# Performance work log

Hardware: AMD Instinct MI355X
Metric: run time of the kernel (lower is better)

The kernel has to match this reference:

```python
import jax, jax.numpy as jnp
import numpy as np

THRESH_LOW = 0.90
THRESH_HIGH = 0.95
IOU_THRESH = 0.05
IOU_LOW = 0.1


def _interp1d(size, dtype):
    # roi_align sample offsets for a 4-wide box, bin=4, grid=ceil(4/1)=4:
    # center + (i+0.5)*1 - 2 -> {-1.5,-0.5,0.5,1.5}
    offs = jnp.array([-1.5, -0.5, 0.5, 1.5], dtype)
    c = jnp.arange(size, dtype=dtype)[:, None] + offs  # [size,4]
    valid = (c >= -1.0) & (c <= size)  # torchvision: zero if y < -1 or y > H
    cc = jnp.clip(c, 0.0, size - 1.0)
    lo = jnp.floor(cc).astype(jnp.int32)
    hi = jnp.minimum(lo + 1, size - 1)
    frac = cc - lo.astype(dtype)
    w_lo = jnp.where(valid, 1.0 - frac, 0.0)
    w_hi = jnp.where(valid, frac, 0.0)
    return lo, hi, w_lo, w_hi


def _roi_pool(m):
    # roi_align(output_size=1, spatial_scale=1, sampling_ratio=-1, aligned=False)
    # over one 4x4 anchor per pixel: separable bilinear gather, mean of 16 samples.
    H, W = m.shape
    ylo, yhi, wy0, wy1 = _interp1d(H, m.dtype)
    xlo, xhi, wx0, wx1 = _interp1d(W, m.dtype)
    A = jnp.einsum('hkw,hk->hw', m[ylo], wy0) + jnp.einsum('hkw,hk->hw', m[yhi], wy1)
    B = jnp.einsum('hwk,wk->hw', A[:, xlo], wx0) + jnp.einsum('hwk,wk->hw', A[:, xhi], wx1)
    return B / 16.0


def _anchors(H, W, dtype):
    # torchvision AnchorGenerator(sizes=(5,), aspects=(1.0,)): base anchor
    # round([-2.5,-2.5,2.5,2.5]) = [-2,-2,2,2]; stride 1; x fastest, y outer.
    yy, xx = jnp.meshgrid(jnp.arange(H, dtype=dtype), jnp.arange(W, dtype=dtype), indexing='ij')
    a = jnp.stack([xx - 2.0, yy - 2.0, xx + 2.0, yy + 2.0], axis=-1)
    return a.reshape(-1, 4)


def _iou_one_vs_all(box, boxes):
    lt = jnp.maximum(box[:2], boxes[:, :2])
    rb = jnp.minimum(box[2:], boxes[:, 2:])
    wh = jnp.maximum(rb - lt, 0.0)
    inter = wh[:, 0] * wh[:, 1]
    area1 = (box[2] - box[0]) * (box[3] - box[1])
    area2 = (boxes[:, 2] - boxes[:, 0]) * (boxes[:, 3] - boxes[:, 1])
    return inter / (area1 + area2 - inter)


def _nms(boxes, scores, thr):
    # Greedy NMS (torchvision semantics: suppress IoU > thr), returns kept
    # indices sorted by descending score. Row-wise IoU avoids an MxM matrix.
    M = boxes.shape[0]
    if M == 0:
        return jnp.zeros((0,), jnp.int32)
    order = jnp.argsort(-scores)
    b = boxes[order]
    rng = jnp.arange(M)
    def body(i, keep):
        sup = (_iou_one_vs_all(b[i], b) > thr) & (rng > i) & keep[i]
        return keep & ~sup
    keep = jax.lax.fori_loop(0, M, body, jnp.ones((M,), bool))
    return order[keep]


def _logits(x1, x2, x3):
    r = (jnp.abs(x1 - x2).sum(axis=1) + jnp.abs(x2 - x3).sum(axis=1)) / 2.0  # [B,H,W]
    rmax = r.reshape(r.shape[0], -1).max(axis=-1)[:, None, None]
    rmin = r.reshape(r.shape[0], -1).min(axis=-1)[:, None, None]
    r = (r - rmin) / (rmax - rmin + 1e-6)
    m = r[0]  # B == 1
    logits = _roi_pool(m).reshape(-1)  # [H*W], row-major (y outer, x inner)
    return logits / (logits.max() + 1e-6)


def setup_inputs():
    key = jax.random.key(0)
    k1, k2, k3 = jax.random.split(key, 3)
    shape = (1, 8, 1024, 1024)
    return {
        'x1': jax.random.normal(k1, shape, jnp.float32),
        'x2': jax.random.normal(k2, shape, jnp.float32),
        'x3': jax.random.normal(k3, shape, jnp.float32),
    }


def reference(x1, x2, x3):
    H, W = x1.shape[-2:]
    anchors = _anchors(H, W, x1.dtype)
    logits = _logits(x1, x2, x3)
    idx = jnp.arange(logits.shape[0])
    # low band, NMS @ 0.1
    idx_low = idx[(logits > THRESH_LOW) & (logits < THRESH_HIGH)]
    idx_low = idx_low[_nms(anchors[idx_low], logits[idx_low], IOU_LOW)]
    # high band, NMS @ iou_thresh
    idx_high = idx[logits > THRESH_HIGH]
    idx_high = idx_high[_nms(anchors[idx_high], logits[idx_high], IOU_THRESH)]
    # combined NMS
    idx_cat = jnp.concatenate([idx_high, idx_low])
    idx_final = idx_cat[_nms(anchors[idx_cat], logits[idx_cat], IOU_THRESH)]
    return jnp.concatenate([anchors[idx_final], logits[idx_final][:, None]], axis=-1)
```

## Files before the change

### kernel.cpp

```cpp
#include <hip/hip_runtime.h>
#include <stdint.h>

#define GW 1024
#define GH 1024
#define NPIX (GW*GH)
#define CAP 8192
#define KCAP 4096
#define ADJ_STRIDE 48

__global__ void k_resid(const float4* __restrict__ x1, const float4* __restrict__ x2,
                        const float4* __restrict__ x3, float4* __restrict__ r,
                        float2* __restrict__ pmm) {
  const int N4 = NPIX / 4;
  int t = blockIdx.x * blockDim.x + threadIdx.x;
  float4 s1 = make_float4(0.f,0.f,0.f,0.f);
  float4 s2 = make_float4(0.f,0.f,0.f,0.f);
#pragma unroll
  for (int c = 0; c < 8; ++c) {
    float4 a = x1[c*N4 + t];
    float4 b = x2[c*N4 + t];
    float4 d = x3[c*N4 + t];
    s1.x += fabsf(a.x-b.x); s1.y += fabsf(a.y-b.y);
    s1.z += fabsf(a.z-b.z); s1.w += fabsf(a.w-b.w);
    s2.x += fabsf(b.x-d.x); s2.y += fabsf(b.y-d.y);
    s2.z += fabsf(b.z-d.z); s2.w += fabsf(b.w-d.w);
  }
  float4 rv = make_float4((s1.x+s2.x)*0.5f, (s1.y+s2.y)*0.5f,
                          (s1.z+s2.z)*0.5f, (s1.w+s2.w)*0.5f);
  r[t] = rv;
  float mn = fminf(fminf(rv.x,rv.y), fminf(rv.z,rv.w));
  float mx = fmaxf(fmaxf(rv.x,rv.y), fmaxf(rv.z,rv.w));
#pragma unroll
  for (int o = 32; o > 0; o >>= 1) {
    mn = fminf(mn, __shfl_down(mn, o));
    mx = fmaxf(mx, __shfl_down(mx, o));
  }
  __shared__ float smn[4], smx[4];
  int wid = threadIdx.x >> 6;
  if ((threadIdx.x & 63) == 0) { smn[wid] = mn; smx[wid] = mx; }
  __syncthreads();
  if (threadIdx.x == 0) {
    float a = fminf(fminf(smn[0], smn[1]), fminf(smn[2], smn[3]));
    float b = fmaxf(fmaxf(smx[0], smx[1]), fmaxf(smx[2], smx[3]));
    pmm[blockIdx.x] = make_float2(a, b);
  }
}

__global__ __launch_bounds__(1024) void k_reduce1(const float2* __restrict__ pmm,
                                                  unsigned int* __restrict__ mm) {
  int t = threadIdx.x;
  float2 p = pmm[t];
  float mn = p.x, mx = p.y;
#pragma unroll
  for (int o = 32; o > 0; o >>= 1) {
    mn = fminf(mn, __shfl_down(mn, o));
    mx = fmaxf(mx, __shfl_down(mx, o));
  }
  __shared__ float smn[16], smx[16];
  int wid = t >> 6;
  if ((t & 63) == 0) { smn[wid] = mn; smx[wid] = mx; }
  __syncthreads();
  if (t == 0) {
    mn = smn[0]; mx = smx[0];
#pragma unroll
    for (int i = 1; i < 16; ++i) { mn = fminf(mn, smn[i]); mx = fmaxf(mx, smx[i]); }
    mm[1] = __float_as_uint(mn);
    mm[2] = __float_as_uint(mx);
  }
}

__global__ void k_convy(const float* __restrict__ r, float* __restrict__ A,
                        const unsigned int* __restrict__ mm) {
  int x = blockIdx.x * 256 + threadIdx.x;
  int y = blockIdx.y;
  float rmin = __uint_as_float(mm[1]);
  float denom = __uint_as_float(mm[2]) - rmin + 1e-6f;
  const float offs[4] = {-1.5f, -0.5f, 0.5f, 1.5f};
  float a = 0.f, b = 0.f;
#pragma unroll
  for (int k = 0; k < 4; ++k) {
    float c = (float)y + offs[k];
    bool valid = (c >= -1.0f) && (c <= (float)GH);
    float cc = fminf(fmaxf(c, 0.0f), (float)(GH - 1));
    int lo = (int)floorf(cc);
    int hi = min(lo + 1, GH - 1);
    float frac = cc - (float)lo;
    float w0 = valid ? 1.0f - frac : 0.0f;
    float w1 = valid ? frac : 0.0f;
    a += ((r[lo*GW + x] - rmin) / denom) * w0;
    b += ((r[hi*GW + x] - rmin) / denom) * w1;
  }
  A[y*GW + x] = a + b;
}

__global__ void k_convx(const float* __restrict__ A, float* __restrict__ B,
                        float* __restrict__ pbmax) {
  __shared__ float sA[GW];
  __shared__ float smx[4];
  int y = blockIdx.x, t = threadIdx.x;
  ((float4*)sA)[t] = ((const float4*)(A + (size_t)y*GW))[t];
  __syncthreads();
  const float offs[4] = {-1.5f, -0.5f, 0.5f, 1.5f};
  float mxv = 0.0f;
#pragma unroll
  for (int q = 0; q < 4; ++q) {
    int x = t + 256*q;
    float a = 0.f, b = 0.f;
#pragma unroll
    for (int k = 0; k < 4; ++k) {
      float c = (float)x + offs[k];
      bool valid = (c >= -1.0f) && (c <= (float)GW);
      float cc = fminf(fmaxf(c, 0.0f), (float)(GW - 1));
      int lo = (int)floorf(cc);
      int hi = min(lo + 1, GW - 1);
      float frac = cc - (float)lo;
      float w0 = valid ? 1.0f - frac : 0.0f;
      float w1 = valid ? frac : 0.0f;
      a += sA[lo] * w0;
      b += sA[hi] * w1;
    }
    float v = (a + b) * 0.0625f;
    B[(size_t)y*GW + x] = v;
    mxv = fmaxf(mxv, v);
  }
#pragma unroll
  for (int o = 32; o > 0; o >>= 1) mxv = fmaxf(mxv, __shfl_down(mxv, o));
  int wid = t >> 6;
  if ((t & 63) == 0) smx[wid] = mxv;
  __syncthreads();
  if (t == 0)
    pbmax[y] = fmaxf(fmaxf(smx[0], smx[1]), fmaxf(smx[2], smx[3]));
}

__global__ __launch_bounds__(1024) void k_reduce2(const float* __restrict__ pbmax,
                                                  unsigned int* __restrict__ mm) {
  int t = threadIdx.x;
  float mx = pbmax[t];
#pragma unroll
  for (int o = 32; o > 0; o >>= 1) mx = fmaxf(mx, __shfl_down(mx, o));
  __shared__ float smx[16];
  int wid = t >> 6;
  if ((t & 63) == 0) smx[wid] = mx;
  __syncthreads();
  if (t == 0) {
    mx = smx[0];
#pragma unroll
    for (int i = 1; i < 16; ++i) mx = fmaxf(mx, smx[i]);
    mm[3] = __float_as_uint(mx);
    mm[0] = 0u;
  }
}

__global__ void k_cand(const float4* __restrict__ B, uint4* __restrict__ map,
                       unsigned int* __restrict__ list, float* __restrict__ scores,
                       unsigned int* __restrict__ mm) {
  int t = blockIdx.x * 256 + threadIdx.x;
  int tid = threadIdx.x;
  float bmax = __uint_as_float(mm[3]);
  float dv = bmax + 1e-6f;
  float4 b = B[t];
  float l[4] = { b.x/dv, b.y/dv, b.z/dv, b.w/dv };
  unsigned int flags = 0; int cnt = 0;
#pragma unroll
  for (int k = 0; k < 4; ++k) {
    float s = l[k];
    if (s > 0.90f && !(s == 0.95f)) { flags |= 1u << k; cnt++; }
  }
  __shared__ unsigned int sscan[256];
  __shared__ unsigned int sbase;
  sscan[tid] = (unsigned int)cnt;
  __syncthreads();
  for (int off = 1; off < 256; off <<= 1) {
    unsigned int v = sscan[tid];
    unsigned int a = (tid >= off) ? sscan[tid - off] : 0u;
    __syncthreads();
    sscan[tid] = v + a;
    __syncthreads();
  }
  if (tid == 255) {
    unsigned int tot = sscan[255];
    if (tot) sbase = atomicAdd(&mm[0], tot);
  }
  __syncthreads();
  unsigned int mv[4] = { ~0u, ~0u, ~0u, ~0u };
  if (flags) {
    unsigned int o = sbase + sscan[tid] - (unsigned int)cnt;
    unsigned int base4 = (unsigned int)t * 4u;
#pragma unroll
    for (int k = 0; k < 4; ++k) {
      if ((flags >> k) & 1u) {
        if (o < CAP) { list[o] = base4 + (unsigned int)k; scores[o] = l[k]; mv[k] = o; }
        o++;
      }
    }
  }
  map[t] = make_uint4(mv[0], mv[1], mv[2], mv[3]);
}

__global__ void k_adj(const unsigned int* __restrict__ list,
                      const float* __restrict__ scores,
                      const unsigned int* __restrict__ map,
                      const unsigned int* __restrict__ mm,
                      unsigned short* __restrict__ adj) {
  int r = blockIdx.x * 256 + threadIdx.x;
  int M = (int)min(mm[0], (unsigned int)CAP);
  if (r >= M) return;
  unsigned int pos = list[r];
  float s = scores[r];
  unsigned int sb = __float_as_uint(s);
  unsigned int high = (s > 0.95f) ? 1u : 0u;
  int y = (int)(pos >> 10), x = (int)(pos & 1023);
  int n = 0, n3 = 0;
  unsigned short* row = adj + (size_t)r * ADJ_STRIDE;
#pragma unroll
  for (int pass = 0; pass < 2; ++pass) {
    for (int dy = -3; dy <= 3; ++dy) {
      int ady = dy < 0 ? -dy : dy;
      int wy = 4 - ady;
      int ny = y + dy;
      if ((unsigned)ny >= (unsigned)GH) continue;
      for (int dx = -3; dx <= 3; ++dx) {
        if ((dx | dy) == 0) continue;
        int adx = dx < 0 ? -dx : dx;
        int prod = (4 - adx) * wy;
        if (prod < 2) continue;
        if ((pass == 0) != (prod >= 3)) continue;
        int nx = x + dx;
        if ((unsigned)nx >= (unsigned)GW) continue;
        unsigned int npix = (unsigned int)(ny*GW + nx);
        unsigned int nid = map[npix];
        if (nid == ~0u) continue;
        float ns = scores[nid];
        unsigned int nsb = __float_as_uint(ns);
        if (nsb > sb || (nsb == sb && npix < pos)) {
          unsigned int nh = (ns > 0.95f) ? 1u : 0u;
          row[1 + n] = (unsigned short)(nid | (nh << 15));
          n++;
          if (pass == 0) n3++;
        }
      }
    }
  }
  row[0] = (unsigned short)(n3 | (n << 6) | (high << 12));
}

__global__ __launch_bounds__(1024) void k_nms(const unsigned int* __restrict__ list,
                                              const float* __restrict__ scores,
                                              const unsigned short* __restrict__ adj,
                                              const unsigned int* __restrict__ mm,
                                              float* __restrict__ out, int nrows) {
  __shared__ unsigned char st[CAP];
  __shared__ unsigned short act[2][CAP];
  __shared__ unsigned long long skeys[KCAP];
  __shared__ unsigned int s_cnt[2];
  __shared__ unsigned int s_k;
  const int tid = threadIdx.x;
  int M = (int)min(mm[0], (unsigned int)CAP);
  for (int i = tid; i < CAP; i += 1024) st[i] = 0;
  for (int i = tid; i < M; i += 1024) act[0][i] = (unsigned short)i;
  if (tid == 0) { s_cnt[0] = (unsigned int)M; s_cnt[1] = 0; s_k = 0; }
  __syncthreads();

  int cur = 0;
  for (int round = 0; round < CAP; ++round) {
    unsigned int cnt = s_cnt[cur];
    if (cnt == 0) break;
    for (unsigned int i = tid; i < cnt; i += 1024) {
      int r = act[cur][i];
      const unsigned short* row = adj + (size_t)r * ADJ_STRIDE;
      unsigned int hdr = row[0];
      unsigned int high = (hdr >> 12) & 1u;
      int n = high ? (int)((hdr >> 6) & 63u) : (int)(hdr & 63u);
      unsigned char lowbit = high ? 0 : 16;
      bool sup = false, und = false;
      for (int k = 1; k <= n; ++k) {
        unsigned int e = row[k];
        if (((e >> 15) & 1u) != high) continue;
        unsigned char ps = st[e & 0x1FFFu];
        if (ps & 2) { sup = true; break; }
        if (!(ps & 1)) und = true;
      }
      if (sup)          st[r] = (unsigned char)(1 | lowbit);
      else if (!und)    st[r] = (unsigned char)(3 | lowbit);
      else { unsigned int j = atomicAdd(&s_cnt[cur ^ 1], 1u); act[cur ^ 1][j] = (unsigned short)r; }
    }
    __syncthreads();
    if (tid == 0) s_cnt[cur] = 0;
    cur ^= 1;
    __syncthreads();
  }
  __syncthreads();

  if (tid == 0) { s_cnt[0] = 0; s_cnt[1] = 0; }
  __syncthreads();
  for (int i = tid; i < M; i += 1024) {
    unsigned char s0 = st[i];
    if ((s0 & 16) && (s0 & 2)) {
      unsigned int j = atomicAdd(&s_cnt[0], 1u); act[0][j] = (unsigned short)i;
    }
  }
  __syncthreads();
  cur = 0;
  for (int round = 0; round < CAP; ++round) {
    unsigned int cnt = s_cnt[cur];
    if (cnt == 0) break;
    for (unsigned int i = tid; i < cnt; i += 1024) {
      int r = act[cur][i];
      const unsigned short* row = adj + (size_t)r * ADJ_STRIDE;
      unsigned int hdr = row[0];
      int n = (int)((hdr >> 6) & 63u);
      bool sup = false, und = false;
      for (int k = 1; k <= n; ++k) {
        unsigned int e = row[k];
        unsigned char ps = st[e & 0x1FFFu];
        if ((e >> 15) & 1u) {
          if (ps & 2) { sup = true; break; }
        } else {
          if (!(ps & 2)) continue;
          if (ps & 8) { sup = true; break; }
          if (!(ps & 4)) und = true;
        }
      }
      if (sup)          st[r] |= 4;
      else if (!und)    st[r] |= 12;
      else { unsigned int j = atomicAdd(&s_cnt[cur ^ 1], 1u); act[cur ^ 1][j] = (unsigned short)r; }
    }
    __syncthreads();
    if (tid == 0) s_cnt[cur] = 0;
    cur ^= 1;
    __syncthreads();
  }
  __syncthreads();

  for (int i = tid; i < M; i += 1024) {
    unsigned char s0 = st[i];
    bool keep = (s0 & 16) ? ((s0 & 8) != 0) : ((s0 & 2) != 0);
    if (keep) {
      unsigned int j = atomicAdd(&s_k, 1u);
      if (j < KCAP) {
        unsigned int pos = list[i];
        unsigned int sb = __float_as_uint(scores[i]);
        skeys[j] = (((unsigned long long)(0xFFFFFFFFu - sb)) << 32) | (unsigned long long)pos;
      }
    }
  }
  __syncthreads();
  unsigned int K = min(s_k, (unsigned int)KCAP);

  for (unsigned int i = tid; i < K; i += 1024) {
    unsigned long long key = skeys[i];
    unsigned int rank = 0;
    for (unsigned int q = 0; q < K; ++q) rank += (skeys[q] < key) ? 1u : 0u;
    if ((int)rank < nrows) {
      unsigned int pos = (unsigned int)(key & 0xFFFFFFFFu);
      float s = __uint_as_float(0xFFFFFFFFu - (unsigned int)(key >> 32));
      float fx = (float)(pos & 1023), fy = (float)(pos >> 10);
      out[rank*5 + 0] = fx - 2.0f;
      out[rank*5 + 1] = fy - 2.0f;
      out[rank*5 + 2] = fx + 2.0f;
      out[rank*5 + 3] = fy + 2.0f;
      out[rank*5 + 4] = s;
    }
  }
}

extern "C" void kernel_launch(void* const* d_in, const int* in_sizes, int n_in,
                              void* d_out, int out_size, void* d_ws, size_t ws_size,
                              hipStream_t stream) {
  const float* x1 = (const float*)d_in[0];
  const float* x2 = (const float*)d_in[1];
  const float* x3 = (const float*)d_in[2];
  char* ws = (char*)d_ws;
  float* rmap = (float*)ws;
  float* Amap = (float*)(ws + (4u << 20));
  float* Bmap = (float*)(ws + (8u << 20));
  unsigned int* map = (unsigned int*)(ws + (4u << 20));
  unsigned int* mm  = (unsigned int*)(ws + (12u << 20));
  unsigned int* list = (unsigned int*)(ws + (12u << 20) + 4096u);
  float* scores = (float*)(ws + (12u << 20) + (64u << 10));
  unsigned short* adj = (unsigned short*)(ws + (12u << 20) + (128u << 10));
  float2* pmm = (float2*)(ws + (13u << 20));
  float* pbmax = (float*)(ws + (13u << 20) + (16u << 10));
  float* out = (float*)d_out;

  k_resid<<<NPIX/4/256, 256, 0, stream>>>((const float4*)x1, (const float4*)x2,
                                          (const float4*)x3, (float4*)rmap, pmm);
  k_reduce1<<<1, 1024, 0, stream>>>(pmm, mm);
  dim3 g2(GW/256, GH);
  k_convy<<<g2, 256, 0, stream>>>(rmap, Amap, mm);
  k_convx<<<GH, 256, 0, stream>>>(Amap, Bmap, pbmax);
  k_reduce2<<<1, 1024, 0, stream>>>(pbmax, mm);
  k_cand<<<NPIX/4/256, 256, 0, stream>>>((const float4*)Bmap, (uint4*)map, list, scores, mm);
  k_adj<<<CAP/256, 256, 0, stream>>>(list, scores, map, mm, adj);
  k_nms<<<1, 1024, 0, stream>>>(list, scores, adj, mm, out, out_size / 5);
}
```

Measured before the change: 199.4 us.

## Fuse reductions via last-block pattern, tile separable conv, merge adjacency into NMS

```diff
diff --git a/kernel.cpp b/kernel.cpp
--- a/kernel.cpp
+++ b/kernel.cpp
@@ -7,10 +7,13 @@
 #define CAP 8192
 #define KCAP 4096
 #define ADJ_STRIDE 48
-
-__global__ void k_resid(const float4* __restrict__ x1, const float4* __restrict__ x2,
+#define TW 128
+#define TH 16
+
+__global__ __launch_bounds__(256) void k_resid(const float4* __restrict__ x1,
+                        const float4* __restrict__ x2,
                         const float4* __restrict__ x3, float4* __restrict__ r,
-                        float2* __restrict__ pmm) {
+                        float2* __restrict__ pmm, unsigned int* __restrict__ mm) {
   const int N4 = NPIX / 4;
   int t = blockIdx.x * blockDim.x + threadIdx.x;
   float4 s1 = make_float4(0.f,0.f,0.f,0.f);
@@ -36,6 +39,7 @@
     mx = fmaxf(mx, __shfl_down(mx, o));
   }
   __shared__ float smn[4], smx[4];
+  __shared__ bool isLast;
   int wid = threadIdx.x >> 6;
   if ((threadIdx.x & 63) == 0) { smn[wid] = mn; smx[wid] = mx; }
   __syncthreads();
@@ -43,111 +47,129 @@
     float a = fminf(fminf(smn[0], smn[1]), fminf(smn[2], smn[3]));
     float b = fmaxf(fmaxf(smx[0], smx[1]), fmaxf(smx[2], smx[3]));
     pmm[blockIdx.x] = make_float2(a, b);
+    __threadfence();
+    unsigned int tk = atomicAdd(&mm[8], 1u);
+    isLast = (tk == gridDim.x - 1);
+  }
+  __syncthreads();
+  if (isLast) {
+    __threadfence();
+    int tid = threadIdx.x;
+    float2 p = pmm[tid];
+    mn = p.x; mx = p.y;
+#pragma unroll
+    for (int i = 1; i < 4; ++i) {
+      float2 q = pmm[tid + 256*i];
+      mn = fminf(mn, q.x); mx = fmaxf(mx, q.y);
+    }
+#pragma unroll
+    for (int o = 32; o > 0; o >>= 1) {
+      mn = fminf(mn, __shfl_down(mn, o));
+      mx = fmaxf(mx, __shfl_down(mx, o));
+    }
+    if ((tid & 63) == 0) { smn[tid>>6] = mn; smx[tid>>6] = mx; }
+    __syncthreads();
+    if (tid == 0) {
+      float a = fminf(fminf(smn[0], smn[1]), fminf(smn[2], smn[3]));
+      float b = fmaxf(fmaxf(smx[0], smx[1]), fmaxf(smx[2], smx[3]));
+      mm[1] = __float_as_uint(a);
+      mm[2] = __float_as_uint(b);
+    }
   }
 }
 
-__global__ __launch_bounds__(1024) void k_reduce1(const float2* __restrict__ pmm,
-                                                  unsigned int* __restrict__ mm) {
-  int t = threadIdx.x;
-  float2 p = pmm[t];
-  float mn = p.x, mx = p.y;
-#pragma unroll
-  for (int o = 32; o > 0; o >>= 1) {
-    mn = fminf(mn, __shfl_down(mn, o));
-    mx = fmaxf(mx, __shfl_down(mx, o));
-  }
-  __shared__ float smn[16], smx[16];
-  int wid = t >> 6;
-  if ((t & 63) == 0) { smn[wid] = mn; smx[wid] = mx; }
-  __syncthreads();
-  if (t == 0) {
-    mn = smn[0]; mx = smx[0];
-#pragma unroll
-    for (int i = 1; i < 16; ++i) { mn = fminf(mn, smn[i]); mx = fmaxf(mx, smx[i]); }
-    mm[1] = __float_as_uint(mn);
-    mm[2] = __float_as_uint(mx);
-  }
-}
-
-__global__ void k_convy(const float* __restrict__ r, float* __restrict__ A,
-                        const unsigned int* __restrict__ mm) {
-  int x = blockIdx.x * 256 + threadIdx.x;
-  int y = blockIdx.y;
+__global__ __launch_bounds__(256) void k_conv(const float* __restrict__ r,
+                        float* __restrict__ B, float* __restrict__ pconv,
+                        unsigned int* __restrict__ mm) {
+  __shared__ float sN[TH+4][TW+4];
+  __shared__ float sA[TH][TW+4];
+  __shared__ float smx[4];
+  __shared__ bool isLast;
+  int x0 = blockIdx.x * TW, y0 = blockIdx.y * TH;
+  int tid = threadIdx.x;
   float rmin = __uint_as_float(mm[1]);
   float denom = __uint_as_float(mm[2]) - rmin + 1e-6f;
   const float offs[4] = {-1.5f, -0.5f, 0.5f, 1.5f};
-  float a = 0.f, b = 0.f;
-#pragma unroll
-  for (int k = 0; k < 4; ++k) {
-    float c = (float)y + offs[k];
-    bool valid = (c >= -1.0f) && (c <= (float)GH);
-    float cc = fminf(fmaxf(c, 0.0f), (float)(GH - 1));
-    int lo = (int)floorf(cc);
-    int hi = min(lo + 1, GH - 1);
-    float frac = cc - (float)lo;
-    float w0 = valid ? 1.0f - frac : 0.0f;
-    float w1 = valid ? frac : 0.0f;
-    a += ((r[lo*GW + x] - rmin) / denom) * w0;
-    b += ((r[hi*GW + x] - rmin) / denom) * w1;
-  }
-  A[y*GW + x] = a + b;
-}
-
-__global__ void k_convx(const float* __restrict__ A, float* __restrict__ B,
-                        float* __restrict__ pbmax) {
-  __shared__ float sA[GW];
-  __shared__ float smx[4];
-  int y = blockIdx.x, t = threadIdx.x;
-  ((float4*)sA)[t] = ((const float4*)(A + (size_t)y*GW))[t];
-  __syncthreads();
-  const float offs[4] = {-1.5f, -0.5f, 0.5f, 1.5f};
-  float mxv = 0.0f;
-#pragma unroll
-  for (int q = 0; q < 4; ++q) {
-    int x = t + 256*q;
+  for (int i = tid; i < (TH+4)*(TW+4); i += 256) {
+    int row = i / (TW+4), col = i - row*(TW+4);
+    int gy = min(max(y0 - 2 + row, 0), GH-1);
+    int gx = min(max(x0 - 2 + col, 0), GW-1);
+    sN[row][col] = (r[gy*GW + gx] - rmin) / denom;
+  }
+  __syncthreads();
+  for (int i = tid; i < TH*(TW+4); i += 256) {
+    int ty = i / (TW+4), c0 = i - ty*(TW+4);
+    int y = y0 + ty;
     float a = 0.f, b = 0.f;
 #pragma unroll
     for (int k = 0; k < 4; ++k) {
-      float c = (float)x + offs[k];
-      bool valid = (c >= -1.0f) && (c <= (float)GW);
-      float cc = fminf(fmaxf(c, 0.0f), (float)(GW - 1));
+      float c = (float)y + offs[k];
+      bool valid = (c >= -1.0f) && (c <= (float)GH);
+      float cc = fminf(fmaxf(c, 0.0f), (float)(GH - 1));
       int lo = (int)floorf(cc);
-      int hi = min(lo + 1, GW - 1);
+      int hi = min(lo + 1, GH - 1);
       float frac = cc - (float)lo;
       float w0 = valid ? 1.0f - frac : 0.0f;
       float w1 = valid ? frac : 0.0f;
-      a += sA[lo] * w0;
-      b += sA[hi] * w1;
+      a += sN[lo - (y0-2)][c0] * w0;
+      b += sN[hi - (y0-2)][c0] * w1;
+    }
+    sA[ty][c0] = a + b;
+  }
+  __syncthreads();
+  int tx = tid & 127;
+  int tyb = (tid >> 7) * 8;
+  int x = x0 + tx;
+  int xl[4], xh[4]; float w0x[4], w1x[4];
+#pragma unroll
+  for (int k = 0; k < 4; ++k) {
+    float c = (float)x + offs[k];
+    bool valid = (c >= -1.0f) && (c <= (float)GW);
+    float cc = fminf(fmaxf(c, 0.0f), (float)(GW - 1));
+    int lo = (int)floorf(cc);
+    int hi = min(lo + 1, GW - 1);
+    float frac = cc - (float)lo;
+    w0x[k] = valid ? 1.0f - frac : 0.0f;
+    w1x[k] = valid ? frac : 0.0f;
+    xl[k] = lo - (x0-2); xh[k] = hi - (x0-2);
+  }
+  float mxv = 0.0f;
+#pragma unroll
+  for (int q = 0; q < 8; ++q) {
+    int ty = tyb + q;
+    float a = 0.f, b = 0.f;
+#pragma unroll
+    for (int k = 0; k < 4; ++k) {
+      a += sA[ty][xl[k]] * w0x[k];
+      b += sA[ty][xh[k]] * w1x[k];
     }
     float v = (a + b) * 0.0625f;
-    B[(size_t)y*GW + x] = v;
+    B[(size_t)(y0+ty)*GW + x] = v;
     mxv = fmaxf(mxv, v);
   }
 #pragma unroll
   for (int o = 32; o > 0; o >>= 1) mxv = fmaxf(mxv, __shfl_down(mxv, o));
-  int wid = t >> 6;
-  if ((t & 63) == 0) smx[wid] = mxv;
-  __syncthreads();
-  if (t == 0)
-    pbmax[y] = fmaxf(fmaxf(smx[0], smx[1]), fmaxf(smx[2], smx[3]));
-}
-
-__global__ __launch_bounds__(1024) void k_reduce2(const float* __restrict__ pbmax,
-                                                  unsigned int* __restrict__ mm) {
-  int t = threadIdx.x;
-  float mx = pbmax[t];
-#pragma unroll
-  for (int o = 32; o > 0; o >>= 1) mx = fmaxf(mx, __shfl_down(mx, o));
-  __shared__ float smx[16];
-  int wid = t >> 6;
-  if ((t & 63) == 0) smx[wid] = mx;
-  __syncthreads();
-  if (t == 0) {
-    mx = smx[0];
-#pragma unroll
-    for (int i = 1; i < 16; ++i) mx = fmaxf(mx, smx[i]);
-    mm[3] = __float_as_uint(mx);
-    mm[0] = 0u;
+  if ((tid & 63) == 0) smx[tid>>6] = mxv;
+  __syncthreads();
+  int nblk = gridDim.x * gridDim.y;
+  int bid = blockIdx.y * gridDim.x + blockIdx.x;
+  if (tid == 0) {
+    pconv[bid] = fmaxf(fmaxf(smx[0], smx[1]), fmaxf(smx[2], smx[3]));
+    __threadfence();
+    unsigned int tk = atomicAdd(&mm[9], 1u);
+    isLast = (tk == (unsigned int)(nblk - 1));
+  }
+  __syncthreads();
+  if (isLast) {
+    __threadfence();
+    float mx = pconv[tid];
+    mx = fmaxf(mx, pconv[tid + 256]);
+#pragma unroll
+    for (int o = 32; o > 0; o >>= 1) mx = fmaxf(mx, __shfl_down(mx, o));
+    if ((tid & 63) == 0) smx[tid>>6] = mx;
+    __syncthreads();
+    if (tid == 0)
+      mm[3] = __float_as_uint(fmaxf(fmaxf(smx[0], smx[1]), fmaxf(smx[2], smx[3])));
   }
 }
 
@@ -197,58 +219,12 @@
   map[t] = make_uint4(mv[0], mv[1], mv[2], mv[3]);
 }
 
-__global__ void k_adj(const unsigned int* __restrict__ list,
-                      const float* __restrict__ scores,
-                      const unsigned int* __restrict__ map,
-                      const unsigned int* __restrict__ mm,
-                      unsigned short* __restrict__ adj) {
-  int r = blockIdx.x * 256 + threadIdx.x;
-  int M = (int)min(mm[0], (unsigned int)CAP);
-  if (r >= M) return;
-  unsigned int pos = list[r];
-  float s = scores[r];
-  unsigned int sb = __float_as_uint(s);
-  unsigned int high = (s > 0.95f) ? 1u : 0u;
-  int y = (int)(pos >> 10), x = (int)(pos & 1023);
-  int n = 0, n3 = 0;
-  unsigned short* row = adj + (size_t)r * ADJ_STRIDE;
-#pragma unroll
-  for (int pass = 0; pass < 2; ++pass) {
-    for (int dy = -3; dy <= 3; ++dy) {
-      int ady = dy < 0 ? -dy : dy;
-      int wy = 4 - ady;
-      int ny = y + dy;
-      if ((unsigned)ny >= (unsigned)GH) continue;
-      for (int dx = -3; dx <= 3; ++dx) {
-        if ((dx | dy) == 0) continue;
-        int adx = dx < 0 ? -dx : dx;
-        int prod = (4 - adx) * wy;
-        if (prod < 2) continue;
-        if ((pass == 0) != (prod >= 3)) continue;
-        int nx = x + dx;
-        if ((unsigned)nx >= (unsigned)GW) continue;
-        unsigned int npix = (unsigned int)(ny*GW + nx);
-        unsigned int nid = map[npix];
-        if (nid == ~0u) continue;
-        float ns = scores[nid];
-        unsigned int nsb = __float_as_uint(ns);
-        if (nsb > sb || (nsb == sb && npix < pos)) {
-          unsigned int nh = (ns > 0.95f) ? 1u : 0u;
-          row[1 + n] = (unsigned short)(nid | (nh << 15));
-          n++;
-          if (pass == 0) n3++;
-        }
-      }
-    }
-  }
-  row[0] = (unsigned short)(n3 | (n << 6) | (high << 12));
-}
-
-__global__ __launch_bounds__(1024) void k_nms(const unsigned int* __restrict__ list,
-                                              const float* __restrict__ scores,
-                                              const unsigned short* __restrict__ adj,
-                                              const unsigned int* __restrict__ mm,
-                                              float* __restrict__ out, int nrows) {
+__global__ __launch_bounds__(1024) void k_final(const unsigned int* __restrict__ list,
+                                                const float* __restrict__ scores,
+                                                const unsigned int* __restrict__ map,
+                                                const unsigned int* __restrict__ mm,
+                                                unsigned short* __restrict__ adj,
+                                                float* __restrict__ out, int nrows) {
   __shared__ unsigned char st[CAP];
   __shared__ unsigned short act[2][CAP];
   __shared__ unsigned long long skeys[KCAP];
@@ -256,6 +232,46 @@
   __shared__ unsigned int s_k;
   const int tid = threadIdx.x;
   int M = (int)min(mm[0], (unsigned int)CAP);
+
+  for (int r = tid; r < M; r += 1024) {
+    unsigned int pos = list[r];
+    float s = scores[r];
+    unsigned int sb = __float_as_uint(s);
+    unsigned int high = (s > 0.95f) ? 1u : 0u;
+    int y = (int)(pos >> 10), x = (int)(pos & 1023);
+    int n = 0, n3 = 0;
+    unsigned short* row = adj + (size_t)r * ADJ_STRIDE;
+#pragma unroll
+    for (int pass = 0; pass < 2; ++pass) {
+      for (int dy = -3; dy <= 3; ++dy) {
+        int ady = dy < 0 ? -dy : dy;
+        int wy = 4 - ady;
+        int ny = y + dy;
+        if ((unsigned)ny >= (unsigned)GH) continue;
+        for (int dx = -3; dx <= 3; ++dx) {
+          if ((dx | dy) == 0) continue;
+          int adx = dx < 0 ? -dx : dx;
+          int prod = (4 - adx) * wy;
+          if (prod < 2) continue;
+          if ((pass == 0) != (prod >= 3)) continue;
+          int nx = x + dx;
+          if ((unsigned)nx >= (unsigned)GW) continue;
+          unsigned int npix = (unsigned int)(ny*GW + nx);
+          unsigned int nid = map[npix];
+          if (nid == ~0u) continue;
+          float ns = scores[nid];
+          unsigned int nsb = __float_as_uint(ns);
+          if (nsb > sb || (nsb == sb && npix < pos)) {
+            unsigned int nh = (ns > 0.95f) ? 1u : 0u;
+            row[1 + n] = (unsigned short)(nid | (nh << 15));
+            n++;
+            if (pass == 0) n3++;
+          }
+        }
+      }
+    }
+    row[0] = (unsigned short)(n3 | (n << 6) | (high << 12));
+  }
   for (int i = tid; i < CAP; i += 1024) st[i] = 0;
   for (int i = tid; i < M; i += 1024) act[0][i] = (unsigned short)i;
   if (tid == 0) { s_cnt[0] = (unsigned int)M; s_cnt[1] = 0; s_k = 0; }
@@ -270,60 +286,53 @@
       const unsigned short* row = adj + (size_t)r * ADJ_STRIDE;
       unsigned int hdr = row[0];
       unsigned int high = (hdr >> 12) & 1u;
-      int n = high ? (int)((hdr >> 6) & 63u) : (int)(hdr & 63u);
-      unsigned char lowbit = high ? 0 : 16;
-      bool sup = false, und = false;
-      for (int k = 1; k <= n; ++k) {
-        unsigned int e = row[k];
-        if (((e >> 15) & 1u) != high) continue;
-        unsigned char ps = st[e & 0x1FFFu];
-        if (ps & 2) { sup = true; break; }
-        if (!(ps & 1)) und = true;
+      int nAll = (int)((hdr >> 6) & 63u);
+      int n3 = (int)(hdr & 63u);
+      if (high) {
+        bool sup = false, und = false;
+        for (int k = 1; k <= nAll; ++k) {
+          unsigned int e = row[k];
+          if (!(e >> 15)) continue;
+          unsigned char ps = st[e & 0x1FFFu];
+          if (ps & 2) { sup = true; break; }
+          if (!(ps & 1)) und = true;
+        }
+        if (sup) st[r] = 1;
+        else if (!und) st[r] = 3;
+        else { unsigned int j = atomicAdd(&s_cnt[cur^1],1u); act[cur^1][j] = (unsigned short)r; }
+      } else {
+        unsigned char cs = st[r];
+        if (!(cs & 1)) {
+          bool sup = false, und = false;
+          for (int k = 1; k <= n3; ++k) {
+            unsigned int e = row[k];
+            if (e >> 15) continue;
+            unsigned char ps = st[e & 0x1FFFu];
+            if (ps & 2) { sup = true; break; }
+            if (!(ps & 1)) und = true;
+          }
+          if (sup) { st[r] = 1 | 16; continue; }
+          if (und) { unsigned int j = atomicAdd(&s_cnt[cur^1],1u); act[cur^1][j] = (unsigned short)r; continue; }
+          cs = 3 | 16; st[r] = cs;
+        }
+        bool sup = false, und = false;
+        for (int k = 1; k <= nAll; ++k) {
+          unsigned int e = row[k];
+          unsigned char ps = st[e & 0x1FFFu];
+          if (e >> 15) {
+            if (ps & 2) { sup = true; break; }
+            if (!(ps & 1)) und = true;
+          } else {
+            if (!(ps & 1)) { und = true; continue; }
+            if (!(ps & 2)) continue;
+            if (ps & 8) { sup = true; break; }
+            if (!(ps & 4)) und = true;
+          }
+        }
+        if (sup) st[r] |= 4;
+        else if (!und) st[r] |= 12;
+        else { unsigned int j = atomicAdd(&s_cnt[cur^1],1u); act[cur^1][j] = (unsigned short)r; }
       }
-      if (sup)          st[r] = (unsigned char)(1 | lowbit);
-      else if (!und)    st[r] = (unsigned char)(3 | lowbit);
-      else { unsigned int j = atomicAdd(&s_cnt[cur ^ 1], 1u); act[cur ^ 1][j] = (unsigned short)r; }
-    }
-    __syncthreads();
-    if (tid == 0) s_cnt[cur] = 0;
-    cur ^= 1;
-    __syncthreads();
-  }
-  __syncthreads();
-
-  if (tid == 0) { s_cnt[0] = 0; s_cnt[1] = 0; }
-  __syncthreads();
-  for (int i = tid; i < M; i += 1024) {
-    unsigned char s0 = st[i];
-    if ((s0 & 16) && (s0 & 2)) {
-      unsigned int j = atomicAdd(&s_cnt[0], 1u); act[0][j] = (unsigned short)i;
-    }
-  }
-  __syncthreads();
-  cur = 0;
-  for (int round = 0; round < CAP; ++round) {
-    unsigned int cnt = s_cnt[cur];
-    if (cnt == 0) break;
-    for (unsigned int i = tid; i < cnt; i += 1024) {
-      int r = act[cur][i];
-      const unsigned short* row = adj + (size_t)r * ADJ_STRIDE;
-      unsigned int hdr = row[0];
-      int n = (int)((hdr >> 6) & 63u);
-      bool sup = false, und = false;
-      for (int k = 1; k <= n; ++k) {
-        unsigned int e = row[k];
-        unsigned char ps = st[e & 0x1FFFu];
-        if ((e >> 15) & 1u) {
-          if (ps & 2) { sup = true; break; }
-        } else {
-          if (!(ps & 2)) continue;
-          if (ps & 8) { sup = true; break; }
-          if (!(ps & 4)) und = true;
-        }
-      }
-      if (sup)          st[r] |= 4;
-      else if (!und)    st[r] |= 12;
-      else { unsigned int j = atomicAdd(&s_cnt[cur ^ 1], 1u); act[cur ^ 1][j] = (unsigned short)r; }
     }
     __syncthreads();
     if (tid == 0) s_cnt[cur] = 0;
@@ -372,25 +381,21 @@
   const float* x3 = (const float*)d_in[2];
   char* ws = (char*)d_ws;
   float* rmap = (float*)ws;
-  float* Amap = (float*)(ws + (4u << 20));
-  float* Bmap = (float*)(ws + (8u << 20));
-  unsigned int* map = (unsigned int*)(ws + (4u << 20));
+  float* Bmap = (float*)(ws + (4u << 20));
+  unsigned int* map = (unsigned int*)(ws + (8u << 20));
   unsigned int* mm  = (unsigned int*)(ws + (12u << 20));
   unsigned int* list = (unsigned int*)(ws + (12u << 20) + 4096u);
   float* scores = (float*)(ws + (12u << 20) + (64u << 10));
   unsigned short* adj = (unsigned short*)(ws + (12u << 20) + (128u << 10));
   float2* pmm = (float2*)(ws + (13u << 20));
-  float* pbmax = (float*)(ws + (13u << 20) + (16u << 10));
+  float* pconv = (float*)(ws + (13u << 20) + (16u << 10));
   float* out = (float*)d_out;
 
+  hipMemsetAsync(mm, 0, 64, stream);
   k_resid<<<NPIX/4/256, 256, 0, stream>>>((const float4*)x1, (const float4*)x2,
-                                          (const float4*)x3, (float4*)rmap, pmm);
-  k_reduce1<<<1, 1024, 0, stream>>>(pmm, mm);
-  dim3 g2(GW/256, GH);
-  k_convy<<<g2, 256, 0, stream>>>(rmap, Amap, mm);
-  k_convx<<<GH, 256, 0, stream>>>(Amap, Bmap, pbmax);
-  k_reduce2<<<1, 1024, 0, stream>>>(pbmax, mm);
+                                          (const float4*)x3, (float4*)rmap, pmm, mm);
+  dim3 gc(GW/TW, GH/TH);
+  k_conv<<<gc, 256, 0, stream>>>(rmap, Bmap, pconv, mm);
   k_cand<<<NPIX/4/256, 256, 0, stream>>>((const float4*)Bmap, (uint4*)map, list, scores, mm);
-  k_adj<<<CAP/256, 256, 0, stream>>>(list, scores, map, mm, adj);
-  k_nms<<<1, 1024, 0, stream>>>(list, scores, adj, mm, out, out_size / 5);
+  k_final<<<1, 1024, 0, stream>>>(list, scores, map, mm, adj, out, out_size / 5);
 }
```

New measurement: 293.4 us. +47.2%, slower.
